# Optimization experiments

Measured on AMD Instinct MI355X. Metric: run time of the kernel, lower is better.

## Reference

```python
import jax, jax.numpy as jnp
import numpy as np

NS, NV = 48, 10            # scalar / vector multiplicities
IN_SIZE = NS + 3*NV + 3*NV + NS   # 156
N_EDGE_FEAT = 96
HIDDEN = 96
# weight shapes per output irrep: 0e:(58,48) 1o:(68,10) 1e:(68,10) 0o:(58,48)
W_SHAPES = [('0e', NS + NV, NS), ('1o', NS + 2*NV, NV), ('1e', 2*NV + NS, NV), ('0o', NV + NS, NS)]
WEIGHT_NUMEL = sum(a*b for _, a, b in W_SHAPES)  # 6928
N_NODES, N_EDGES = 10000, 50000


def setup_inputs() -> dict:
    key = jax.random.key(0)
    ks = jax.random.split(key, 9)
    node_attr = jax.random.normal(ks[0], (N_NODES, IN_SIZE), dtype=jnp.float32)
    edge_index = jax.random.randint(ks[1], (2, N_EDGES), 0, N_NODES)
    edge_attr = jax.random.normal(ks[2], (N_EDGES, N_EDGE_FEAT), dtype=jnp.float32)
    edge_sh = jax.random.normal(ks[3], (N_EDGES, 4), dtype=jnp.float32)
    s1 = 1.0 / np.sqrt(N_EDGE_FEAT)
    s2 = 1.0 / np.sqrt(HIDDEN)
    W1 = jax.random.normal(ks[4], (N_EDGE_FEAT, HIDDEN), dtype=jnp.float32) * s1
    b1 = jnp.zeros((HIDDEN,), dtype=jnp.float32)
    W2 = jax.random.normal(ks[5], (HIDDEN, WEIGHT_NUMEL), dtype=jnp.float32) * s2
    b2 = jnp.zeros((WEIGHT_NUMEL,), dtype=jnp.float32)
    return {'node_attr': node_attr, 'edge_index': edge_index, 'edge_attr': edge_attr,
            'edge_sh': edge_sh, 'W1': W1, 'b1': b1, 'W2': W2, 'b2': b2}


def _faster_tp(in_, sh, weight):
    # in_: [E, 156], sh: [E, 4], weight: [E, 6928]
    in_0e = in_[:, :NS]                                   # [E,48]
    in_1o = in_[:, NS:NS + 3*NV].reshape(-1, NV, 3)       # [E,10,3]
    in_1e = in_[:, NS + 3*NV:NS + 6*NV].reshape(-1, NV, 3)
    in_0o = in_[:, NS + 6*NV:]                            # [E,48]
    sh_0e = sh[:, 0]                                      # [E]
    sh_1o = sh[:, 1:]                                     # [E,3]
    inv_s3 = 1.0 / np.sqrt(3.0)
    inv_s2 = 1.0 / np.sqrt(2.0)

    out_0e = jnp.concatenate([
        in_0e * sh_0e[:, None],
        jnp.sum(in_1o * sh_1o[:, None, :], axis=-1) * inv_s3], axis=-1)      # [E,58]
    out_1o = jnp.concatenate([
        in_0e[:, :, None] * sh_1o[:, None, :],
        in_1o * sh_0e[:, None, None],
        jnp.cross(in_1e, sh_1o[:, None, :]) * inv_s2], axis=-2)              # [E,68,3]
    out_1e = jnp.concatenate([
        jnp.cross(in_1o, sh_1o[:, None, :]) * inv_s2,
        in_1e * sh_0e[:, None, None],
        in_0o[:, :, None] * sh_1o[:, None, :]], axis=-2)                     # [E,68,3]
    out_0o = jnp.concatenate([
        jnp.sum(in_1e * sh_1o[:, None, :], axis=-1) * inv_s3,
        in_0o * sh_0e[:, None]], axis=-1)                                    # [E,58]

    wd = {}
    start = 0
    for name, a, b in W_SHAPES:
        wd[name] = weight[:, start:start + a*b].reshape(-1, a, b) / np.sqrt(a)
        start += a*b

    o0e = jnp.einsum('ei,eio->eo', out_0e, wd['0e'])                 # [E,48]
    o1o = jnp.einsum('eic,eio->eoc', out_1o, wd['1o']).reshape(-1, 3*NV)
    o1e = jnp.einsum('eic,eio->eoc', out_1e, wd['1e']).reshape(-1, 3*NV)
    o0o = jnp.einsum('ei,eio->eo', out_0o, wd['0o'])                 # [E,48]
    return jnp.concatenate([o0e, o1o, o1e, o0o], axis=-1)           # [E,156]


def reference(node_attr, edge_index, edge_attr, edge_sh, W1, b1, W2, b2):
    edge_src, edge_dst = edge_index[0], edge_index[1]
    # edge MLP -> per-edge TP weights
    h = jax.nn.relu(edge_attr @ W1 + b1)
    w = h @ W2 + b2                                       # [E, 6928]
    tp = _faster_tp(node_attr[edge_dst], edge_sh, w)      # [E, 156]
    # scatter-mean over source nodes
    n = node_attr.shape[0]
    seg = jax.ops.segment_sum(tp, edge_src, num_segments=n)
    cnt = jax.ops.segment_sum(jnp.ones((tp.shape[0],), tp.dtype), edge_src, num_segments=n)
    out = seg / jnp.maximum(cnt, 1.0)[:, None]
    # residual (in/out sizes equal, so pad is a no-op)
    return out + node_attr
```

## Files before the change

kernel.cpp:

```cpp
#include <hip/hip_runtime.h>

#define NE 50000
#define NN 10000
#define KH 96
#define KE 128
#define WN 6928
#define WP 7744
#define NTILE 484
#define IN_SZ 156
#define EPW 32

typedef __attribute__((ext_vector_type(8))) short short8;
typedef __attribute__((ext_vector_type(4))) float float4v;

__device__ __forceinline__ unsigned short f2bf(float x) {
  unsigned u = __float_as_uint(x);
  unsigned r = (u + 0x7FFFu + ((u >> 16) & 1u)) >> 16;
  return (unsigned short)r;
}
__device__ __forceinline__ float b2f(unsigned short u) {
  return __uint_as_float(((unsigned)u) << 16);
}

__device__ __forceinline__ void issue4(short8 (&B)[4], const unsigned short* p) {
  asm volatile("global_load_dwordx4 %0, %4, off\n\t"
               "global_load_dwordx4 %1, %4, off offset:1024\n\t"
               "global_load_dwordx4 %2, %4, off offset:2048\n\t"
               "global_load_dwordx4 %3, %4, off offset:3072"
               : "=&v"(B[0]), "=&v"(B[1]), "=&v"(B[2]), "=&v"(B[3])
               : "v"(p));
}
__device__ __forceinline__ void wait4(short8 (&B)[4]) {
  asm volatile("s_waitcnt vmcnt(4)"
               : "+v"(B[0]), "+v"(B[1]), "+v"(B[2]), "+v"(B[3]));
}
__device__ __forceinline__ void wait0(short8 (&B)[4]) {
  asm volatile("s_waitcnt vmcnt(0)"
               : "+v"(B[0]), "+v"(B[1]), "+v"(B[2]), "+v"(B[3]));
}

__global__ __launch_bounds__(256) void cast_kernel(
    const float* __restrict__ edge_attr, const float* __restrict__ W1,
    unsigned short* __restrict__ ea_bf, unsigned short* __restrict__ W1T)
{
  int idx = blockIdx.x * 256 + threadIdx.x;
  const int nea = NE * KH / 8;
  if (idx < nea) {
    const float* p = edge_attr + (size_t)idx * 8;
    float4 x = *(const float4*)p, y = *(const float4*)(p + 4);
    uint4 pk;
    pk.x = f2bf(x.x) | ((unsigned)f2bf(x.y) << 16);
    pk.y = f2bf(x.z) | ((unsigned)f2bf(x.w) << 16);
    pk.z = f2bf(y.x) | ((unsigned)f2bf(y.y) << 16);
    pk.w = f2bf(y.z) | ((unsigned)f2bf(y.w) << 16);
    *(uint4*)(ea_bf + (size_t)idx * 8) = pk;
  } else {
    int j = idx - nea;
    if (j < KH * KH) {
      int c = j / KH, k = j - c * KH;
      W1T[c * KH + k] = f2bf(W1[k * KH + c]);
    }
  }
}

__global__ __launch_bounds__(384) void mlp1_kernel(
    const unsigned short* __restrict__ ea_bf, const unsigned short* __restrict__ W1T,
    const float* __restrict__ b1, unsigned short* __restrict__ h_ext)
{
  const int tid = threadIdx.x;
  const int e0 = blockIdx.x * 16;
  const int w = tid >> 6, l = tid & 15, q = (tid >> 4) & 3;

  short8 a[3], b[3];
  #pragma unroll
  for (int s = 0; s < 3; ++s) {
    a[s] = *(const short8*)(ea_bf + (size_t)(e0 + l) * KH + s * 32 + q * 8);
    b[s] = *(const short8*)(W1T + (size_t)(w * 16 + l) * KH + s * 32 + q * 8);
  }
  float4v C = {0.f, 0.f, 0.f, 0.f};
  #pragma unroll
  for (int s = 0; s < 3; ++s)
    C = __builtin_amdgcn_mfma_f32_16x16x32_bf16(a[s], b[s], C, 0, 0, 0);

  float bv = b1[w * 16 + l];
  #pragma unroll
  for (int r = 0; r < 4; ++r)
    h_ext[(size_t)(e0 + q * 4 + r) * KE + w * 16 + l] = f2bf(fmaxf(C[r] + bv, 0.f));

  for (int idx = tid; idx < 16 * 32; idx += 384) {
    int e = idx >> 5, c = 96 + (idx & 31);
    h_ext[(size_t)(e0 + e) * KE + c] = (c == 96) ? (unsigned short)0x3F80 : (unsigned short)0;
  }
}

__global__ __launch_bounds__(256) void w2pt_kernel(
    const float* __restrict__ W2, const float* __restrict__ b2,
    unsigned short* __restrict__ W2PT)
{
  int gid = blockIdx.x * 256 + threadIdx.x;
  if (gid >= NTILE * 256) return;
  int lane = gid & 63, s = (gid >> 6) & 3, t = gid >> 8;
  int l = lane & 15, q = lane >> 4;
  int np = t * 16 + l;
  int c;
  if (np < 2784) c = np;
  else if (np < 3872) { int rel = np - 2784, i = rel >> 4, o = rel & 15; c = (o < 10) ? 2784 + i * 10 + o : -1; }
  else if (np < 4960) { int rel = np - 3872, i = rel >> 4, o = rel & 15; c = (o < 10) ? 3464 + i * 10 + o : -1; }
  else c = 4144 + (np - 4960);

  int kbase = s * 32 + q * 8;
  unsigned short o8[8];
  #pragma unroll
  for (int j = 0; j < 8; ++j) {
    int k = kbase + j;
    float v = 0.f;
    if (c >= 0) v = (k < KH) ? W2[(size_t)k * WN + c] : (k == KH ? b2[c] : 0.f);
    o8[j] = f2bf(v);
  }
  uint4 pk;
  pk.x = o8[0] | ((unsigned)o8[1] << 16);
  pk.y = o8[2] | ((unsigned)o8[3] << 16);
  pk.z = o8[4] | ((unsigned)o8[5] << 16);
  pk.w = o8[6] | ((unsigned)o8[7] << 16);
  *(uint4*)(W2PT + (size_t)gid * 8) = pk;
}

__global__ __launch_bounds__(512, 2) void tp_kernel(
    const unsigned short* __restrict__ h_ext, const float* __restrict__ node_attr,
    const int* __restrict__ edge_index, const float* __restrict__ edge_sh,
    const unsigned short* __restrict__ W2PT,
    float* __restrict__ acc, int* __restrict__ icnt)
{
  __shared__ unsigned short sIn[EPW][160];
  __shared__ float sOut[EPW][160];
  __shared__ unsigned short sF0[2][60][EPW];
  __shared__ unsigned short sF1[2][70][3][EPW];
  __shared__ float sShs[EPW][4];
  __shared__ int sSrc[EPW], sDst[EPW];

  const int tid = threadIdx.x;
  const int e0 = blockIdx.x * EPW;

  if (tid < EPW) {
    int ok = (e0 + tid) < NE;
    int s = ok ? edge_index[e0 + tid] : 0;
    int d = ok ? edge_index[NE + e0 + tid] : 0;
    sSrc[tid] = s; sDst[tid] = d;
    if (ok) atomicAdd(&icnt[s], 1);
  }
  if (tid >= 128 && tid < 256) {
    int t2 = tid - 128;
    int e = t2 >> 2, c = t2 & 3;
    sShs[e][c] = ((e0 + e) < NE) ? edge_sh[(size_t)(e0 + e) * 4 + c] : 0.f;
  }
  __syncthreads();

  for (int idx = tid; idx < EPW * IN_SZ; idx += 512) {
    int e = idx / IN_SZ, f = idx - e * IN_SZ;
    sIn[e][f] = f2bf(node_attr[(size_t)sDst[e] * IN_SZ + f]);
  }
  for (int idx = tid; idx < EPW * 160; idx += 512) (&sOut[0][0])[idx] = 0.f;
  __syncthreads();

  {
    const int e = tid >> 4, j = tid & 15;
    const float sh0 = sShs[e][0], sx = sShs[e][1], sy = sShs[e][2], sz = sShs[e][3];
    const float i3 = 0.57735026918962576f, i2 = 0.70710678118654752f;
    for (int i = j; i < 48; i += 16) {
      float v0 = b2f(sIn[e][i]), w0 = b2f(sIn[e][108 + i]);
      sF0[0][i][e] = f2bf(v0 * sh0);
      sF0[1][10 + i][e] = f2bf(w0 * sh0);
      sF1[0][i][0][e] = f2bf(v0 * sx); sF1[0][i][1][e] = f2bf(v0 * sy); sF1[0][i][2][e] = f2bf(v0 * sz);
      sF1[1][20 + i][0][e] = f2bf(w0 * sx); sF1[1][20 + i][1][e] = f2bf(w0 * sy); sF1[1][20 + i][2][e] = f2bf(w0 * sz);
    }
    if (j < 10) {
      const int v = j;
      float ax = b2f(sIn[e][48 + 3 * v]), ay = b2f(sIn[e][48 + 3 * v + 1]), az = b2f(sIn[e][48 + 3 * v + 2]);
      float bx = b2f(sIn[e][78 + 3 * v]), by = b2f(sIn[e][78 + 3 * v + 1]), bz = b2f(sIn[e][78 + 3 * v + 2]);
      sF0[0][48 + v][e] = f2bf((ax * sx + ay * sy + az * sz) * i3);
      sF0[1][v][e]      = f2bf((bx * sx + by * sy + bz * sz) * i3);
      sF1[0][48 + v][0][e] = f2bf(ax * sh0); sF1[0][48 + v][1][e] = f2bf(ay * sh0); sF1[0][48 + v][2][e] = f2bf(az * sh0);
      sF1[0][58 + v][0][e] = f2bf((by * sz - bz * sy) * i2);
      sF1[0][58 + v][1][e] = f2bf((bz * sx - bx * sz) * i2);
      sF1[0][58 + v][2][e] = f2bf((bx * sy - by * sx) * i2);
      sF1[1][v][0][e] = f2bf((ay * sz - az * sy) * i2);
      sF1[1][v][1][e] = f2bf((az * sx - ax * sz) * i2);
      sF1[1][v][2][e] = f2bf((ax * sy - ay * sx) * i2);
      sF1[1][10 + v][0][e] = f2bf(bx * sh0); sF1[1][10 + v][1][e] = f2bf(by * sh0); sF1[1][10 + v][2][e] = f2bf(bz * sh0);
    }
  }
  if (tid < 128) {
    int fam = tid >> 6, i = 58 + ((tid >> 5) & 1), e = tid & 31;
    sF0[fam][i][e] = 0;
  } else if (tid < 128 + 384) {
    int t2 = tid - 128;
    int fam = t2 / 192, r = t2 - fam * 192;
    int i = 68 + (r / 96), r2 = r % 96, cc = r2 >> 5, e = r2 & 31;
    sF1[fam][i][cc][e] = 0;
  }
  __syncthreads();

  const int wv = tid >> 6, l = tid & 15, q = (tid >> 4) & 3;

  short8 Af[2][4];
  #pragma unroll
  for (int m = 0; m < 2; ++m) {
    const unsigned short* ar = h_ext + (size_t)(e0 + m * 16 + l) * KE + q * 8;
    #pragma unroll
    for (int s = 0; s < 4; ++s) Af[m][s] = *(const short8*)(ar + s * 32);
  }

  const unsigned short* wlane = W2PT + (size_t)(tid & 63) * 8;
  short8 Ba[4], Bb[4];

  if (wv < 4) {
    const int sf = wv >> 1;
    const int ibeg = (wv & 1) * 30;
    const int tb = sf ? 310 : 0;
    const int obase = sf ? 108 : 0;
    #pragma unroll 1
    for (int ob = 0; ob < 3; ++ob) {
      float a0[4] = {0.f, 0.f, 0.f, 0.f}, a1[4] = {0.f, 0.f, 0.f, 0.f};
      auto addr = [&](int ii) {
        int i = ibeg + ii; if (i >= 58) i = ibeg;
        return wlane + (size_t)(tb + 3 * i + ob) * 2048;
      };
      auto body = [&](const short8 (&B)[4], int ii) {
        int i = ibeg + ii;
        ushort4 f0 = *(const ushort4*)&sF0[sf][i][q * 4];
        ushort4 f1 = *(const ushort4*)&sF0[sf][i][16 + q * 4];
        float4v C0 = {0.f, 0.f, 0.f, 0.f}, C1 = {0.f, 0.f, 0.f, 0.f};
        #pragma unroll
        for (int s = 0; s < 4; ++s) {
          C0 = __builtin_amdgcn_mfma_f32_16x16x32_bf16(Af[0][s], B[s], C0, 0, 0, 0);
          C1 = __builtin_amdgcn_mfma_f32_16x16x32_bf16(Af[1][s], B[s], C1, 0, 0, 0);
        }
        a0[0] += C0[0] * b2f(f0.x); a0[1] += C0[1] * b2f(f0.y);
        a0[2] += C0[2] * b2f(f0.z); a0[3] += C0[3] * b2f(f0.w);
        a1[0] += C1[0] * b2f(f1.x); a1[1] += C1[1] * b2f(f1.y);
        a1[2] += C1[2] * b2f(f1.z); a1[3] += C1[3] * b2f(f1.w);
      };
      issue4(Ba, addr(0));
      issue4(Bb, addr(1));
      #pragma unroll 1
      for (int ii = 0; ii < 28; ii += 2) {
        wait4(Ba); body(Ba, ii);     issue4(Ba, addr(ii + 2));
        wait4(Bb); body(Bb, ii + 1); issue4(Bb, addr(ii + 3));
      }
      wait4(Ba); body(Ba, 28);
      wait0(Bb); body(Bb, 29);
      const int col = obase + ob * 16 + l;
      #pragma unroll
      for (int r = 0; r < 4; ++r) {
        unsafeAtomicAdd(&sOut[q * 4 + r][col], a0[r]);
        unsafeAtomicAdd(&sOut[16 + q * 4 + r][col], a1[r]);
      }
    }
  } else {
    const int vf = (wv >> 1) - 2;
    const int ibeg = (wv & 1) ? 34 : 0;
    const int N = (wv & 1) ? 36 : 34;
    const int tb = vf ? 242 : 174;
    float r0[4][3] = {{0.f}}, r1[4][3] = {{0.f}};
    auto addr = [&](int ii) {
      int i = ibeg + ii; if (i >= 68) i = ibeg;
      return wlane + (size_t)(tb + i) * 2048;
    };
    auto body = [&](const short8 (&B)[4], int ii) {
      int i = ibeg + ii;
      ushort4 g0[3], g1[3];
      #pragma unroll
      for (int cc = 0; cc < 3; ++cc) {
        g0[cc] = *(const ushort4*)&sF1[vf][i][cc][q * 4];
        g1[cc] = *(const ushort4*)&sF1[vf][i][cc][16 + q * 4];
      }
      float4v C0 = {0.f, 0.f, 0.f, 0.f}, C1 = {0.f, 0.f, 0.f, 0.f};
      #pragma unroll
      for (int s = 0; s < 4; ++s) {
        C0 = __builtin_amdgcn_mfma_f32_16x16x32_bf16(Af[0][s], B[s], C0, 0, 0, 0);
        C1 = __builtin_amdgcn_mfma_f32_16x16x32_bf16(Af[1][s], B[s], C1, 0, 0, 0);
      }
      #pragma unroll
      for (int cc = 0; cc < 3; ++cc) {
        r0[0][cc] += C0[0] * b2f(g0[cc].x); r0[1][cc] += C0[1] * b2f(g0[cc].y);
        r0[2][cc] += C0[2] * b2f(g0[cc].z); r0[3][cc] += C0[3] * b2f(g0[cc].w);
        r1[0][cc] += C1[0] * b2f(g1[cc].x); r1[1][cc] += C1[1] * b2f(g1[cc].y);
        r1[2][cc] += C1[2] * b2f(g1[cc].z); r1[3][cc] += C1[3] * b2f(g1[cc].w);
      }
    };
    issue4(Ba, addr(0));
    issue4(Bb, addr(1));
    #pragma unroll 1
    for (int ii = 0; ii < N - 2; ii += 2) {
      wait4(Ba); body(Ba, ii);     issue4(Ba, addr(ii + 2));
      wait4(Bb); body(Bb, ii + 1); issue4(Bb, addr(ii + 3));
    }
    wait4(Ba); body(Ba, N - 2);
    wait0(Bb); body(Bb, N - 1);
    if (l < 10) {
      const int col = (vf ? 78 : 48) + 3 * l;
      #pragma unroll
      for (int r = 0; r < 4; ++r)
        #pragma unroll
        for (int cc = 0; cc < 3; ++cc) {
          unsafeAtomicAdd(&sOut[q * 4 + r][col + cc], r0[r][cc]);
          unsafeAtomicAdd(&sOut[16 + q * 4 + r][col + cc], r1[r][cc]);
        }
    }
  }
  __syncthreads();

  const float n58 = 0.13130643285972254f, n68 = 0.12126781251816650f;
  for (int idx = tid; idx < EPW * IN_SZ; idx += 512) {
    int e = idx / IN_SZ, o = idx - e * IN_SZ;
    if (e0 + e < NE) {
      float nrm = (o < 48 || o >= 108) ? n58 : n68;
      unsafeAtomicAdd(&acc[(size_t)sSrc[e] * IN_SZ + o], sOut[e][o] * nrm);
    }
  }
}

__global__ __launch_bounds__(256) void finalize_kernel(
    const float* __restrict__ acc, const int* __restrict__ icnt,
    const float* __restrict__ node_attr, float* __restrict__ out)
{
  int idx = blockIdx.x * 256 + threadIdx.x;
  if (idx < NN * IN_SZ) {
    int n = idx / IN_SZ;
    out[idx] = acc[idx] / fmaxf((float)icnt[n], 1.f) + node_attr[idx];
  }
}

extern "C" void kernel_launch(void* const* d_in, const int* in_sizes, int n_in,
                              void* d_out, int out_size, void* d_ws, size_t ws_size,
                              hipStream_t stream)
{
  const float* node_attr  = (const float*)d_in[0];
  const int*   edge_index = (const int*)d_in[1];
  const float* edge_attr  = (const float*)d_in[2];
  const float* edge_sh    = (const float*)d_in[3];
  const float* W1 = (const float*)d_in[4];
  const float* b1 = (const float*)d_in[5];
  const float* W2 = (const float*)d_in[6];
  const float* b2 = (const float*)d_in[7];
  float* out = (float*)d_out;

  unsigned short* h_ext = (unsigned short*)d_ws;
  unsigned short* W2PT  = h_ext + (size_t)50016 * KE;
  unsigned short* ea_bf = W2PT + (size_t)NTILE * 2048;
  unsigned short* W1T   = ea_bf + (size_t)NE * KH;
  float* acc  = (float*)ea_bf;
  int*   icnt = (int*)(W1T + KH * KH + 64);

  cast_kernel<<<(NE * KH / 8 + KH * KH + 255) / 256, 256, 0, stream>>>(edge_attr, W1, ea_bf, W1T);
  w2pt_kernel<<<NTILE, 256, 0, stream>>>(W2, b2, W2PT);
  mlp1_kernel<<<NE / 16, 384, 0, stream>>>(ea_bf, W1T, b1, h_ext);
  hipMemsetAsync(acc, 0, (size_t)NN * IN_SZ * sizeof(float), stream);
  hipMemsetAsync(icnt, 0, (size_t)NN * sizeof(int), stream);
  hipMemsetAsync(h_ext + (size_t)50000 * KE, 0, (size_t)16 * KE * sizeof(unsigned short), stream);
  tp_kernel<<<(NE + EPW - 1) / EPW, 512, 0, stream>>>(h_ext, node_attr, edge_index,
                                                      edge_sh, W2PT, acc, icnt);
  finalize_kernel<<<(NN * IN_SZ + 255) / 256, 256, 0, stream>>>(acc, icnt, node_attr, out);
}
```

Measured before the change: 326.6 us.

## Fuse prep kernels and memsets, cast edge_attr in MLP1, triple-buffer weight loads

Merges the W2 repack, W1 transpose and all zeroing memsets into one prep kernel, and drops the separate edge_attr bf16 cast pass by converting inside mlp1. In the TP kernel, weight tiles are now triple-buffered with deeper vmcnt waits, node gathers use float4 loads, and the scalar features stay fp32 in shared memory. The vector-path work split is also rebalanced to 36/36 by padding sF1 to 72 rows. Together these aim to cut launch overhead and extra memory passes and to hide more load latency, at the cost of more registers and LDS per block.

```diff
diff --git a/kernel.cpp b/kernel.cpp
--- a/kernel.cpp
+++ b/kernel.cpp
@@ -5,7 +5,6 @@
 #define KH 96
 #define KE 128
 #define WN 6928
-#define WP 7744
 #define NTILE 484
 #define IN_SZ 156
 #define EPW 32
@@ -30,6 +29,10 @@
                : "=&v"(B[0]), "=&v"(B[1]), "=&v"(B[2]), "=&v"(B[3])
                : "v"(p));
 }
+__device__ __forceinline__ void wait8(short8 (&B)[4]) {
+  asm volatile("s_waitcnt vmcnt(8)"
+               : "+v"(B[0]), "+v"(B[1]), "+v"(B[2]), "+v"(B[3]));
+}
 __device__ __forceinline__ void wait4(short8 (&B)[4]) {
   asm volatile("s_waitcnt vmcnt(4)"
                : "+v"(B[0]), "+v"(B[1]), "+v"(B[2]), "+v"(B[3]));
@@ -39,32 +42,51 @@
                : "+v"(B[0]), "+v"(B[1]), "+v"(B[2]), "+v"(B[3]));
 }
 
-__global__ __launch_bounds__(256) void cast_kernel(
-    const float* __restrict__ edge_attr, const float* __restrict__ W1,
-    unsigned short* __restrict__ ea_bf, unsigned short* __restrict__ W1T)
-{
-  int idx = blockIdx.x * 256 + threadIdx.x;
-  const int nea = NE * KH / 8;
-  if (idx < nea) {
-    const float* p = edge_attr + (size_t)idx * 8;
-    float4 x = *(const float4*)p, y = *(const float4*)(p + 4);
+__global__ __launch_bounds__(256) void prep_kernel(
+    const float* __restrict__ W2, const float* __restrict__ b2,
+    const float* __restrict__ W1,
+    unsigned short* __restrict__ W2PT, unsigned short* __restrict__ W1T,
+    uint4* __restrict__ zbase, unsigned short* __restrict__ h_ext)
+{
+  const int b = blockIdx.x, tid = threadIdx.x;
+  if (b < NTILE) {
+    int lane = tid & 63, s = tid >> 6;
+    int l = lane & 15, q = lane >> 4;
+    int np = b * 16 + l;
+    int c;
+    if (np < 2784) c = np;
+    else if (np < 3872) { int rel = np - 2784, i = rel >> 4, o = rel & 15; c = (o < 10) ? 2784 + i * 10 + o : -1; }
+    else if (np < 4960) { int rel = np - 3872, i = rel >> 4, o = rel & 15; c = (o < 10) ? 3464 + i * 10 + o : -1; }
+    else c = 4144 + (np - 4960);
+    int kbase = s * 32 + q * 8;
+    unsigned short o8[8];
+    #pragma unroll
+    for (int j = 0; j < 8; ++j) {
+      int k = kbase + j;
+      float v = 0.f;
+      if (c >= 0) v = (k < KH) ? W2[(size_t)k * WN + c] : (k == KH ? b2[c] : 0.f);
+      o8[j] = f2bf(v);
+    }
     uint4 pk;
-    pk.x = f2bf(x.x) | ((unsigned)f2bf(x.y) << 16);
-    pk.y = f2bf(x.z) | ((unsigned)f2bf(x.w) << 16);
-    pk.z = f2bf(y.x) | ((unsigned)f2bf(y.y) << 16);
-    pk.w = f2bf(y.z) | ((unsigned)f2bf(y.w) << 16);
-    *(uint4*)(ea_bf + (size_t)idx * 8) = pk;
+    pk.x = o8[0] | ((unsigned)o8[1] << 16);
+    pk.y = o8[2] | ((unsigned)o8[3] << 16);
+    pk.z = o8[4] | ((unsigned)o8[5] << 16);
+    pk.w = o8[6] | ((unsigned)o8[7] << 16);
+    *(uint4*)(W2PT + ((size_t)b * 256 + tid) * 8) = pk;
+  } else if (b < NTILE + 36) {
+    int j = (b - NTILE) * 256 + tid;
+    int c = j / KH, k = j - c * KH;
+    W1T[c * KH + k] = f2bf(W1[k * KH + c]);
+  } else if (b < NTILE + 36 + 1534) {
+    int idx = (b - NTILE - 36) * 256 + tid;
+    if (idx < 392500) zbase[idx] = (uint4){0u, 0u, 0u, 0u};
   } else {
-    int j = idx - nea;
-    if (j < KH * KH) {
-      int c = j / KH, k = j - c * KH;
-      W1T[c * KH + k] = f2bf(W1[k * KH + c]);
-    }
+    ((uint4*)(h_ext + (size_t)50000 * KE))[tid] = (uint4){0u, 0u, 0u, 0u};
   }
 }
 
 __global__ __launch_bounds__(384) void mlp1_kernel(
-    const unsigned short* __restrict__ ea_bf, const unsigned short* __restrict__ W1T,
+    const float* __restrict__ edge_attr, const unsigned short* __restrict__ W1T,
     const float* __restrict__ b1, unsigned short* __restrict__ h_ext)
 {
   const int tid = threadIdx.x;
@@ -72,9 +94,15 @@
   const int w = tid >> 6, l = tid & 15, q = (tid >> 4) & 3;
 
   short8 a[3], b[3];
+  const float* ar = edge_attr + (size_t)(e0 + l) * KH + q * 8;
   #pragma unroll
   for (int s = 0; s < 3; ++s) {
-    a[s] = *(const short8*)(ea_bf + (size_t)(e0 + l) * KH + s * 32 + q * 8);
+    float4 x = *(const float4*)(ar + s * 32);
+    float4 y = *(const float4*)(ar + s * 32 + 4);
+    a[s][0] = (short)f2bf(x.x); a[s][1] = (short)f2bf(x.y);
+    a[s][2] = (short)f2bf(x.z); a[s][3] = (short)f2bf(x.w);
+    a[s][4] = (short)f2bf(y.x); a[s][5] = (short)f2bf(y.y);
+    a[s][6] = (short)f2bf(y.z); a[s][7] = (short)f2bf(y.w);
     b[s] = *(const short8*)(W1T + (size_t)(w * 16 + l) * KH + s * 32 + q * 8);
   }
   float4v C = {0.f, 0.f, 0.f, 0.f};
@@ -91,38 +119,6 @@
     int e = idx >> 5, c = 96 + (idx & 31);
     h_ext[(size_t)(e0 + e) * KE + c] = (c == 96) ? (unsigned short)0x3F80 : (unsigned short)0;
   }
-}
-
-__global__ __launch_bounds__(256) void w2pt_kernel(
-    const float* __restrict__ W2, const float* __restrict__ b2,
-    unsigned short* __restrict__ W2PT)
-{
-  int gid = blockIdx.x * 256 + threadIdx.x;
-  if (gid >= NTILE * 256) return;
-  int lane = gid & 63, s = (gid >> 6) & 3, t = gid >> 8;
-  int l = lane & 15, q = lane >> 4;
-  int np = t * 16 + l;
-  int c;
-  if (np < 2784) c = np;
-  else if (np < 3872) { int rel = np - 2784, i = rel >> 4, o = rel & 15; c = (o < 10) ? 2784 + i * 10 + o : -1; }
-  else if (np < 4960) { int rel = np - 3872, i = rel >> 4, o = rel & 15; c = (o < 10) ? 3464 + i * 10 + o : -1; }
-  else c = 4144 + (np - 4960);
-
-  int kbase = s * 32 + q * 8;
-  unsigned short o8[8];
-  #pragma unroll
-  for (int j = 0; j < 8; ++j) {
-    int k = kbase + j;
-    float v = 0.f;
-    if (c >= 0) v = (k < KH) ? W2[(size_t)k * WN + c] : (k == KH ? b2[c] : 0.f);
-    o8[j] = f2bf(v);
-  }
-  uint4 pk;
-  pk.x = o8[0] | ((unsigned)o8[1] << 16);
-  pk.y = o8[2] | ((unsigned)o8[3] << 16);
-  pk.z = o8[4] | ((unsigned)o8[5] << 16);
-  pk.w = o8[6] | ((unsigned)o8[7] << 16);
-  *(uint4*)(W2PT + (size_t)gid * 8) = pk;
 }
 
 __global__ __launch_bounds__(512, 2) void tp_kernel(
@@ -133,8 +129,8 @@
 {
   __shared__ unsigned short sIn[EPW][160];
   __shared__ float sOut[EPW][160];
-  __shared__ unsigned short sF0[2][60][EPW];
-  __shared__ unsigned short sF1[2][70][3][EPW];
+  __shared__ float sF0[2][60][EPW];
+  __shared__ unsigned short sF1[2][72][3][EPW];
   __shared__ float sShs[EPW][4];
   __shared__ int sSrc[EPW], sDst[EPW];
 
@@ -155,9 +151,12 @@
   }
   __syncthreads();
 
-  for (int idx = tid; idx < EPW * IN_SZ; idx += 512) {
-    int e = idx / IN_SZ, f = idx - e * IN_SZ;
-    sIn[e][f] = f2bf(node_attr[(size_t)sDst[e] * IN_SZ + f]);
+  for (int idx = tid; idx < EPW * 39; idx += 512) {
+    int e = idx / 39, f4 = idx - e * 39;
+    float4 x = *(const float4*)(node_attr + (size_t)sDst[e] * IN_SZ + f4 * 4);
+    ushort4 u;
+    u.x = f2bf(x.x); u.y = f2bf(x.y); u.z = f2bf(x.z); u.w = f2bf(x.w);
+    *(ushort4*)&sIn[e][f4 * 4] = u;
   }
   for (int idx = tid; idx < EPW * 160; idx += 512) (&sOut[0][0])[idx] = 0.f;
   __syncthreads();
@@ -168,8 +167,8 @@
     const float i3 = 0.57735026918962576f, i2 = 0.70710678118654752f;
     for (int i = j; i < 48; i += 16) {
       float v0 = b2f(sIn[e][i]), w0 = b2f(sIn[e][108 + i]);
-      sF0[0][i][e] = f2bf(v0 * sh0);
-      sF0[1][10 + i][e] = f2bf(w0 * sh0);
+      sF0[0][i][e] = v0 * sh0;
+      sF0[1][10 + i][e] = w0 * sh0;
       sF1[0][i][0][e] = f2bf(v0 * sx); sF1[0][i][1][e] = f2bf(v0 * sy); sF1[0][i][2][e] = f2bf(v0 * sz);
       sF1[1][20 + i][0][e] = f2bf(w0 * sx); sF1[1][20 + i][1][e] = f2bf(w0 * sy); sF1[1][20 + i][2][e] = f2bf(w0 * sz);
     }
@@ -177,8 +176,8 @@
       const int v = j;
       float ax = b2f(sIn[e][48 + 3 * v]), ay = b2f(sIn[e][48 + 3 * v + 1]), az = b2f(sIn[e][48 + 3 * v + 2]);
       float bx = b2f(sIn[e][78 + 3 * v]), by = b2f(sIn[e][78 + 3 * v + 1]), bz = b2f(sIn[e][78 + 3 * v + 2]);
-      sF0[0][48 + v][e] = f2bf((ax * sx + ay * sy + az * sz) * i3);
-      sF0[1][v][e]      = f2bf((bx * sx + by * sy + bz * sz) * i3);
+      sF0[0][48 + v][e] = (ax * sx + ay * sy + az * sz) * i3;
+      sF0[1][v][e]      = (bx * sx + by * sy + bz * sz) * i3;
       sF1[0][48 + v][0][e] = f2bf(ax * sh0); sF1[0][48 + v][1][e] = f2bf(ay * sh0); sF1[0][48 + v][2][e] = f2bf(az * sh0);
       sF1[0][58 + v][0][e] = f2bf((by * sz - bz * sy) * i2);
       sF1[0][58 + v][1][e] = f2bf((bz * sx - bx * sz) * i2);
@@ -191,11 +190,11 @@
   }
   if (tid < 128) {
     int fam = tid >> 6, i = 58 + ((tid >> 5) & 1), e = tid & 31;
-    sF0[fam][i][e] = 0;
-  } else if (tid < 128 + 384) {
-    int t2 = tid - 128;
-    int fam = t2 / 192, r = t2 - fam * 192;
-    int i = 68 + (r / 96), r2 = r % 96, cc = r2 >> 5, e = r2 & 31;
+    sF0[fam][i][e] = 0.f;
+  }
+  for (int idx = tid; idx < 768; idx += 512) {
+    int fam = idx / 384, r = idx - fam * 384;
+    int i = 68 + r / 96, r2 = r % 96, cc = r2 >> 5, e = r2 & 31;
     sF1[fam][i][cc][e] = 0;
   }
   __syncthreads();
@@ -211,7 +210,7 @@
   }
 
   const unsigned short* wlane = W2PT + (size_t)(tid & 63) * 8;
-  short8 Ba[4], Bb[4];
+  short8 Ba[4], Bb[4], Bc[4];
 
   if (wv < 4) {
     const int sf = wv >> 1;
@@ -227,28 +226,27 @@
       };
       auto body = [&](const short8 (&B)[4], int ii) {
         int i = ibeg + ii;
-        ushort4 f0 = *(const ushort4*)&sF0[sf][i][q * 4];
-        ushort4 f1 = *(const ushort4*)&sF0[sf][i][16 + q * 4];
+        float4 f0 = *(const float4*)&sF0[sf][i][q * 4];
+        float4 f1 = *(const float4*)&sF0[sf][i][16 + q * 4];
         float4v C0 = {0.f, 0.f, 0.f, 0.f}, C1 = {0.f, 0.f, 0.f, 0.f};
         #pragma unroll
         for (int s = 0; s < 4; ++s) {
           C0 = __builtin_amdgcn_mfma_f32_16x16x32_bf16(Af[0][s], B[s], C0, 0, 0, 0);
           C1 = __builtin_amdgcn_mfma_f32_16x16x32_bf16(Af[1][s], B[s], C1, 0, 0, 0);
         }
-        a0[0] += C0[0] * b2f(f0.x); a0[1] += C0[1] * b2f(f0.y);
-        a0[2] += C0[2] * b2f(f0.z); a0[3] += C0[3] * b2f(f0.w);
-        a1[0] += C1[0] * b2f(f1.x); a1[1] += C1[1] * b2f(f1.y);
-        a1[2] += C1[2] * b2f(f1.z); a1[3] += C1[3] * b2f(f1.w);
+        a0[0] += C0[0] * f0.x; a0[1] += C0[1] * f0.y; a0[2] += C0[2] * f0.z; a0[3] += C0[3] * f0.w;
+        a1[0] += C1[0] * f1.x; a1[1] += C1[1] * f1.y; a1[2] += C1[2] * f1.z; a1[3] += C1[3] * f1.w;
       };
-      issue4(Ba, addr(0));
-      issue4(Bb, addr(1));
+      issue4(Ba, addr(0)); issue4(Bb, addr(1)); issue4(Bc, addr(2));
       #pragma unroll 1
-      for (int ii = 0; ii < 28; ii += 2) {
-        wait4(Ba); body(Ba, ii);     issue4(Ba, addr(ii + 2));
-        wait4(Bb); body(Bb, ii + 1); issue4(Bb, addr(ii + 3));
-      }
-      wait4(Ba); body(Ba, 28);
-      wait0(Bb); body(Bb, 29);
+      for (int ii = 0; ii < 27; ii += 3) {
+        wait8(Ba); body(Ba, ii);     issue4(Ba, addr(ii + 3));
+        wait8(Bb); body(Bb, ii + 1); issue4(Bb, addr(ii + 4));
+        wait8(Bc); body(Bc, ii + 2); issue4(Bc, addr(ii + 5));
+      }
+      wait8(Ba); body(Ba, 27);
+      wait4(Bb); body(Bb, 28);
+      wait0(Bc); body(Bc, 29);
       const int col = obase + ob * 16 + l;
       #pragma unroll
       for (int r = 0; r < 4; ++r) {
@@ -258,8 +256,7 @@
     }
   } else {
     const int vf = (wv >> 1) - 2;
-    const int ibeg = (wv & 1) ? 34 : 0;
-    const int N = (wv & 1) ? 36 : 34;
+    const int ibeg = (wv & 1) * 36;
     const int tb = vf ? 242 : 174;
     float r0[4][3] = {{0.f}}, r1[4][3] = {{0.f}};
     auto addr = [&](int ii) {
@@ -288,15 +285,16 @@
         r1[2][cc] += C1[2] * b2f(g1[cc].z); r1[3][cc] += C1[3] * b2f(g1[cc].w);
       }
     };
-    issue4(Ba, addr(0));
-    issue4(Bb, addr(1));
+    issue4(Ba, addr(0)); issue4(Bb, addr(1)); issue4(Bc, addr(2));
     #pragma unroll 1
-    for (int ii = 0; ii < N - 2; ii += 2) {
-      wait4(Ba); body(Ba, ii);     issue4(Ba, addr(ii + 2));
-      wait4(Bb); body(Bb, ii + 1); issue4(Bb, addr(ii + 3));
-    }
-    wait4(Ba); body(Ba, N - 2);
-    wait0(Bb); body(Bb, N - 1);
+    for (int ii = 0; ii < 33; ii += 3) {
+      wait8(Ba); body(Ba, ii);     issue4(Ba, addr(ii + 3));
+      wait8(Bb); body(Bb, ii + 1); issue4(Bb, addr(ii + 4));
+      wait8(Bc); body(Bc, ii + 2); issue4(Bc, addr(ii + 5));
+    }
+    wait8(Ba); body(Ba, 33);
+    wait4(Bb); body(Bb, 34);
+    wait0(Bc); body(Bc, 35);
     if (l < 10) {
       const int col = (vf ? 78 : 48) + 3 * l;
       #pragma unroll
@@ -347,17 +345,13 @@
 
   unsigned short* h_ext = (unsigned short*)d_ws;
   unsigned short* W2PT  = h_ext + (size_t)50016 * KE;
-  unsigned short* ea_bf = W2PT + (size_t)NTILE * 2048;
-  unsigned short* W1T   = ea_bf + (size_t)NE * KH;
-  float* acc  = (float*)ea_bf;
-  int*   icnt = (int*)(W1T + KH * KH + 64);
-
-  cast_kernel<<<(NE * KH / 8 + KH * KH + 255) / 256, 256, 0, stream>>>(edge_attr, W1, ea_bf, W1T);
-  w2pt_kernel<<<NTILE, 256, 0, stream>>>(W2, b2, W2PT);
-  mlp1_kernel<<<NE / 16, 384, 0, stream>>>(ea_bf, W1T, b1, h_ext);
-  hipMemsetAsync(acc, 0, (size_t)NN * IN_SZ * sizeof(float), stream);
-  hipMemsetAsync(icnt, 0, (size_t)NN * sizeof(int), stream);
-  hipMemsetAsync(h_ext + (size_t)50000 * KE, 0, (size_t)16 * KE * sizeof(unsigned short), stream);
+  unsigned short* W1T   = W2PT + (size_t)NTILE * 2048;
+  float* acc  = (float*)(W1T + 9216);
+  int*   icnt = (int*)(acc + (size_t)NN * IN_SZ);
+
+  prep_kernel<<<NTILE + 36 + 1534 + 1, 256, 0, stream>>>(W2, b2, W1, W2PT, W1T,
+                                                         (uint4*)acc, h_ext);
+  mlp1_kernel<<<NE / 16, 384, 0, stream>>>(edge_attr, W1T, b1, h_ext);
   tp_kernel<<<(NE + EPW - 1) / EPW, 512, 0, stream>>>(h_ext, node_attr, edge_index,
                                                       edge_sh, W2PT, acc, icnt);
   finalize_kernel<<<(NN * IN_SZ + 255) / 256, 256, 0, stream>>>(acc, icnt, node_attr, out);
```

Result: slower. 352.9 us (+8.0%).
